# Performance work log

Measured on AMD Instinct MI355X. Metric: run time of the kernel, lower is better.

## Reference

```python
import jax, jax.numpy as jnp
import numpy as np

EPS = 1e-6
TEMP_GEO = 0.07
W_LOCAL = 0.5
W_SHARP = 0.5


def _l2norm(x):
    return x / jnp.clip(jnp.linalg.norm(x, axis=-1, keepdims=True), 1e-12)


def setup_inputs() -> dict:
    key = jax.random.key(0)
    ks = jax.random.split(key, 6)
    B, L, S, C = 8, 1024, 1024, 128
    N, P = 8, 256
    q_geo = _l2norm(jax.random.normal(ks[0], (B, L, C), jnp.float32))
    geo_pos = _l2norm(jax.random.normal(ks[1], (B, S, C), jnp.float32))
    label = jax.random.randint(ks[2], (B, L, S), 0, 2, jnp.int32)
    q_cl = jax.random.normal(ks[3], (N, P, C), jnp.float32)
    cl_pos = jax.random.normal(ks[4], (N, P, C), jnp.float32)
    idx = jax.random.randint(ks[5], (N,), 0, P, jnp.int32)
    return {"q_geo": q_geo, "q_cl": q_cl, "geo_pos": geo_pos,
            "cl_pos": cl_pos, "label": label, "idx": idx}


def _masked_mean(v, m):
    # per-sample mean over the [L,S] plane of entries where m is True
    m = m.astype(v.dtype)
    return jnp.sum(v * m, axis=(1, 2)) / jnp.maximum(jnp.sum(m, axis=(1, 2)), 1.0)


def _loftr_loss(conf, label):
    # standard LoFTR coarse CE loss (LoFTRLoss source absent from repo snippet)
    conf = jnp.clip(conf, EPS, 1.0 - EPS)
    pos = label == 1
    neg = label == 0
    pos_loss = _masked_mean(-jnp.log(conf), pos)          # [B]
    neg_loss = _masked_mean(-jnp.log(1.0 - conf), neg)    # [B]
    loss = pos_loss + neg_loss
    return jnp.mean(loss), jnp.mean(pos_loss), jnp.mean(neg_loss)


def _geometric_loss(q, k, label):
    sim = jnp.einsum('blc,bsc->bls', q, k) / TEMP_GEO        # [B,L,S]
    conf = jax.nn.softmax(sim, axis=1) * jax.nn.softmax(sim, axis=2)
    return _loftr_loss(conf, label)


def _sharpness_loss(q, k, label):
    sim = (1.0 + jnp.einsum('blc,bsc->bls', q, k)) / 2.0     # [B,L,S]
    # column stats (over L, dim=0 per sample) -> sharpness1 [B,S]
    s1 = (jnp.max(sim, axis=1) - jnp.mean(sim, axis=1)) / jnp.std(sim, axis=1, ddof=1)
    sharp1 = jax.nn.softmax(s1, axis=-1)
    # row stats (over S, dim=1 per sample) -> sharpness2 [B,L]
    s2 = (jnp.max(sim, axis=2) - jnp.mean(sim, axis=2)) / jnp.std(sim, axis=2, ddof=1)
    sharp2 = jax.nn.softmax(s2, axis=-1)
    simc = jnp.clip(sim, EPS, 1.0 - EPS)
    nll = -jnp.log(simc)
    pos = (label == 1).astype(simc.dtype)
    neg = (label == 0)
    loss1 = jnp.sum(nll * sharp1[:, None, :] * pos, axis=(1, 2))   # [B]
    loss2 = jnp.sum(nll * sharp2[:, :, None] * pos, axis=(1, 2))   # [B]
    loss3 = _masked_mean(-jnp.log(1.0 - simc), neg)                # [B]
    losses = (loss1 + loss2) / 2.0 + loss3
    return sharp1, jnp.mean(losses)


def _contrast_loss(q, all_k):
    # intended math of GeCoContrast: full cosine matrix, diag positives, tail negatives
    N = q.shape[0]
    sim = (1.0 + _l2norm(q) @ _l2norm(all_k).T) / 2.0   # [N, M]
    sim = jnp.clip(sim, EPS, 1.0 - EPS)
    l_pos = jnp.diagonal(sim[:, :N])                    # [N]
    l_neg = sim[:, N:]                                  # [N, M-N]
    return (jnp.mean(-jnp.log(l_pos)) + jnp.mean(-jnp.log(1.0 - l_neg))) / 2.0


def _forward(q_geo, q_cl, geo_pos, cl_pos, label, idx):
    loss_geo, geo_pos_loss, geo_neg_loss = _geometric_loss(q_geo, geo_pos, label)
    sharpness, loss_sharp = _sharpness_loss(q_geo, geo_pos, label)
    loss_geo = ((1.0 - W_SHARP) * loss_geo + W_SHARP * loss_sharp) * W_LOCAL

    N, P, C = q_cl.shape
    ar = jnp.arange(N)
    q_sel = q_cl[ar, idx]                               # [N,C]
    sel = cl_pos[ar, idx]                               # [N,C] positives moved to slot 0
    first = cl_pos[:, 0, :]
    swapped = cl_pos.at[ar, idx].set(first).at[:, 0, :].set(sel)
    cl_pos_save = sel
    all_k = jnp.concatenate([swapped[:, 0, :],
                             swapped[:, 1:, :].reshape(N * (P - 1), C)], axis=0)
    loss_cl = _contrast_loss(q_sel, all_k) * (1.0 - W_LOCAL)

    total = loss_geo + loss_cl
    return (sharpness, cl_pos_save, total, geo_pos_loss, geo_neg_loss, loss_sharp, loss_cl)


def reference(q_geo, q_cl, geo_pos, cl_pos, label, idx):
    return _forward(q_geo, q_cl, geo_pos, cl_pos, label, idx)
```

## Files before the change

kernel.cpp:

```cpp
#include <hip/hip_runtime.h>
#include <math.h>

#define BB 8
#define LL 1024
#define SS 1024
#define CC 128
#define NN 8
#define PP 256

static constexpr float EPS       = 1e-6f;
static constexpr float ONE_M_EPS = 1.0f - 1e-6f;
static constexpr float INV_T     = 1.0f / 0.07f;
static constexpr float NLL_MAX   = 13.815511f;
static constexpr float NLL_MIN   = 1.0000005e-6f;

static constexpr size_t DOTSZ      = (size_t)BB * LL * SS;
static constexpr size_t OFF_LSER   = DOTSZ;
static constexpr size_t OFF_LSEC   = DOTSZ + 16384;
static constexpr size_t OFF_SHARP2 = DOTSZ + 32768;
static constexpr size_t OFF_RP     = DOTSZ + 40960;
static constexpr size_t OFF_CP     = OFF_RP + 524288;
static constexpr size_t OFF_ACC    = OFF_CP + 524288;
static constexpr size_t OFF_ACCCL  = OFF_ACC + 48;
static constexpr size_t OFF_QN     = OFF_ACC + 64;
static constexpr size_t OFF_ASP    = OFF_ACC + 2048;
static constexpr size_t OFF_BSP    = OFF_ASP + 1048576;

static constexpr int OUT_CLSAVE = 8192;
static constexpr int OUT_SCAL   = 9216;

typedef __bf16 bf16x8 __attribute__((ext_vector_type(8)));
typedef float  floatx4 __attribute__((ext_vector_type(4)));

__device__ __forceinline__ void split_f4(float4 x,
                                         unsigned& hp0, unsigned& hp1,
                                         unsigned& lp0, unsigned& lp1) {
    unsigned u0 = __builtin_bit_cast(unsigned, x.x);
    unsigned u1 = __builtin_bit_cast(unsigned, x.y);
    unsigned u2 = __builtin_bit_cast(unsigned, x.z);
    unsigned u3 = __builtin_bit_cast(unsigned, x.w);
    unsigned r0 = u0 + 0x7FFFu + ((u0 >> 16) & 1u);
    unsigned r1 = u1 + 0x7FFFu + ((u1 >> 16) & 1u);
    unsigned r2 = u2 + 0x7FFFu + ((u2 >> 16) & 1u);
    unsigned r3 = u3 + 0x7FFFu + ((u3 >> 16) & 1u);
    float s0 = x.x - __builtin_bit_cast(float, r0 & 0xFFFF0000u);
    float s1 = x.y - __builtin_bit_cast(float, r1 & 0xFFFF0000u);
    float s2 = x.z - __builtin_bit_cast(float, r2 & 0xFFFF0000u);
    float s3 = x.w - __builtin_bit_cast(float, r3 & 0xFFFF0000u);
    hp0 = __builtin_amdgcn_perm(r1, r0, 0x07060302u);
    hp1 = __builtin_amdgcn_perm(r3, r2, 0x07060302u);
    lp0 = __builtin_amdgcn_perm(__builtin_bit_cast(unsigned, s1),
                                __builtin_bit_cast(unsigned, s0), 0x07060302u);
    lp1 = __builtin_amdgcn_perm(__builtin_bit_cast(unsigned, s3),
                                __builtin_bit_cast(unsigned, s2), 0x07060302u);
}

__global__ __launch_bounds__(256) void presplit(const float* __restrict__ A,
                                                const float* __restrict__ Bm,
                                                const float* __restrict__ q_cl,
                                                const float* __restrict__ cl_pos,
                                                const int* __restrict__ idx,
                                                float* __restrict__ out,
                                                float* __restrict__ ws) {
    int tid = threadIdx.x;
    if (blockIdx.x == 1024) {
        int lane = tid & 63, w = tid >> 6;
        if (tid < 52) ws[OFF_ACC + tid] = 0.0f;
        for (int n = w; n < NN; n += 4) {
            int in = idx[n];
            const float* q = q_cl + ((size_t)(n * PP + in)) * CC;
            float2 qv = *(const float2*)(q + 2 * lane);
            float ss = qv.x * qv.x + qv.y * qv.y;
            for (int o = 32; o; o >>= 1) ss += __shfl_xor(ss, o);
            float inv = 1.0f / fmaxf(sqrtf(ss), 1e-12f);
            *(float2*)(ws + OFF_QN + n * 128 + 2 * lane) = make_float2(qv.x * inv, qv.y * inv);
            const float* cp = cl_pos + ((size_t)(n * PP + in)) * CC;
            float2 cv = *(const float2*)(cp + 2 * lane);
            *(float2*)(out + OUT_CLSAVE + n * 128 + 2 * lane) = cv;
        }
        return;
    }
    int bb  = blockIdx.x;
    int mat = bb >> 9;
    size_t grow = (size_t)(bb & 511) * 16 + (tid >> 4);
    int c   = tid & 15;
    const float* in = (mat ? Bm : A) + grow * CC + c * 8;
    float4 v0 = *(const float4*)in;
    float4 v1 = *(const float4*)(in + 4);
    unsigned h0, h1, l0, l1, h2, h3, l2, l3;
    split_f4(v0, h0, h1, l0, l1);
    split_f4(v1, h2, h3, l2, l3);
    float* outp = ws + (mat ? OFF_BSP : OFF_ASP) + grow * 128 + (size_t)(c >> 2) * 32 + (c & 3) * 4;
    *(uint4*)outp        = make_uint4(h0, h1, h2, h3);
    *(uint4*)(outp + 16) = make_uint4(l0, l1, l2, l3);
}

__global__ __launch_bounds__(256, 2) void gemm_dot(float* __restrict__ dot,
                                                   float* __restrict__ ws) {
    __shared__ __align__(16) char lds[2][32768];

    int tid  = threadIdx.x;
    int lane = tid & 63;
    int w    = tid >> 6;

    int t  = blockIdx.x;
    int b  = t >> 6;
    int rm = t & 63;
    int bl = rm >> 3, bs = rm & 7;
    int R0 = bl * 128, C0 = bs * 128;

    const float* Ab = ws + OFF_ASP + ((size_t)(b * 1024 + R0)) * 128;
    const float* Bb = ws + OFF_BSP + ((size_t)(b * 1024 + C0)) * 128;

    const float* srcp[8];
    int ldsb[8];
#pragma unroll
    for (int i = 0; i < 8; i++) {
        int g   = i * 256 + tid;
        int mat = g >> 10;
        int r   = (g >> 3) & 127;
        int pc  = g & 7;
        int c   = pc ^ (r & 7);
        srcp[i] = (mat ? Bb : Ab) + (size_t)r * 128 + (c >> 2) * 16 + (c & 3) * 4;
        ldsb[i] = g * 16;
    }

    int fl   = lane & 15;
    int quad = lane >> 4;
    int wr   = w >> 1, wc = w & 1;
    int Rw   = wr * 64, Cw = wc * 64;

    floatx4 acc[4][4];
#pragma unroll
    for (int i = 0; i < 4; i++)
#pragma unroll
        for (int j = 0; j < 4; j++) acc[i][j] = (floatx4){0.f, 0.f, 0.f, 0.f};

    uint4 rg[8];
#pragma unroll
    for (int i = 0; i < 8; i++) rg[i] = *(const uint4*)(srcp[i]);
#pragma unroll
    for (int i = 0; i < 8; i++) *(uint4*)(&lds[0][ldsb[i]]) = rg[i];
    __syncthreads();

    for (int ks = 0; ks < 4; ks++) {
        int cur = ks & 1;
        if (ks < 3) {
#pragma unroll
            for (int i = 0; i < 8; i++)
                rg[i] = *(const uint4*)(srcp[i] + (ks + 1) * 32);
        }
        const char* la = lds[cur];
        const char* lb = lds[cur] + 16384;
        bf16x8 ah[4], al[4];
#pragma unroll
        for (int mt = 0; mt < 4; mt++) {
            int row = Rw + mt * 16 + fl;
            int sw  = row & 7;
            ah[mt] = *(const bf16x8*)(la + row * 128 + ((quad ^ sw) * 16));
            al[mt] = *(const bf16x8*)(la + row * 128 + (((quad + 4) ^ sw) * 16));
        }
#pragma unroll
        for (int nt = 0; nt < 4; nt++) {
            int row = Cw + nt * 16 + fl;
            int sw  = row & 7;
            bf16x8 bh  = *(const bf16x8*)(lb + row * 128 + ((quad ^ sw) * 16));
            bf16x8 blo = *(const bf16x8*)(lb + row * 128 + (((quad + 4) ^ sw) * 16));
#pragma unroll
            for (int mt = 0; mt < 4; mt++) {
                acc[mt][nt] = __builtin_amdgcn_mfma_f32_16x16x32_bf16(ah[mt], bh,  acc[mt][nt], 0, 0, 0);
                acc[mt][nt] = __builtin_amdgcn_mfma_f32_16x16x32_bf16(ah[mt], blo, acc[mt][nt], 0, 0, 0);
                acc[mt][nt] = __builtin_amdgcn_mfma_f32_16x16x32_bf16(al[mt], bh,  acc[mt][nt], 0, 0, 0);
            }
        }
        if (ks < 3) {
            char* nxt = lds[cur ^ 1];
#pragma unroll
            for (int i = 0; i < 8; i++) *(uint4*)(&nxt[ldsb[i]]) = rg[i];
        }
        __syncthreads();
    }

#pragma unroll
    for (int mt = 0; mt < 4; mt++)
#pragma unroll
        for (int nt = 0; nt < 4; nt++) {
            int col = C0 + Cw + nt * 16 + fl;
#pragma unroll
            for (int r = 0; r < 4; r++) {
                int row = R0 + Rw + mt * 16 + quad * 4 + r;
                dot[((size_t)(b * 1024 + row)) * 1024 + col] = acc[mt][nt][r];
            }
        }

    int stile = bs * 2 + wc;
    int ltile = bl * 2 + wr;
    float ces[4], cmx[4], csm[4], csq[4];
#pragma unroll
    for (int nt = 0; nt < 4; nt++) { ces[nt] = 0.f; cmx[nt] = -1e30f; csm[nt] = 0.f; csq[nt] = 0.f; }
#pragma unroll
    for (int mt = 0; mt < 4; mt++) {
#pragma unroll
        for (int r = 0; r < 4; r++) {
            float es = 0.f, mx = -1e30f, sm = 0.f, sq = 0.f;
#pragma unroll
            for (int nt = 0; nt < 4; nt++) {
                float d  = acc[mt][nt][r];
                float e  = __expf(d * INV_T);
                float s2 = fmaf(0.5f, d, 0.5f);
                es += e; mx = fmaxf(mx, s2); sm += s2; sq += s2 * s2;
                ces[nt] += e; cmx[nt] = fmaxf(cmx[nt], s2); csm[nt] += s2; csq[nt] += s2 * s2;
            }
            for (int o = 1; o < 16; o <<= 1) {
                es += __shfl_xor(es, o);
                mx = fmaxf(mx, __shfl_xor(mx, o));
                sm += __shfl_xor(sm, o);
                sq += __shfl_xor(sq, o);
            }
            if (fl == 0) {
                int row = R0 + Rw + mt * 16 + quad * 4 + r;
                *(float4*)(ws + OFF_RP + (((size_t)(b * 16 + stile)) * 1024 + row) * 4) =
                    make_float4(es, mx, sm, sq);
            }
        }
    }
#pragma unroll
    for (int nt = 0; nt < 4; nt++) {
        float es = ces[nt], mx = cmx[nt], sm = csm[nt], sq = csq[nt];
        for (int o = 16; o < 64; o <<= 1) {
            es += __shfl_xor(es, o);
            mx = fmaxf(mx, __shfl_xor(mx, o));
            sm += __shfl_xor(sm, o);
            sq += __shfl_xor(sq, o);
        }
        if (quad == 0) {
            int col = C0 + Cw + nt * 16 + fl;
            *(float4*)(ws + OFF_CP + (((size_t)(b * 16 + ltile)) * 1024 + col) * 4) =
                make_float4(es, mx, sm, sq);
        }
    }
}

__global__ __launch_bounds__(256) void mid(const float* __restrict__ cl_pos,
                                           const int* __restrict__ idx,
                                           float* __restrict__ ws,
                                           float* __restrict__ out) {
    int q   = blockIdx.x;
    int tid = threadIdx.x;
    int lane = tid & 63, wid = tid >> 6;

    if (q < 16) {
        bool docol = (q < 8);
        int b = q & 7;
        const float* part = ws + (docol ? OFF_CP : OFF_RP);
        float* lse = ws + (docol ? OFF_LSEC : OFF_LSER) + (size_t)b * 1024;
        float zs[4];
        float mxall = -1e30f;
#pragma unroll
        for (int r = 0; r < 4; r++) {
            int i = tid + r * 256;
            float es = 0.f, mx = -1e30f, sm = 0.f, sq = 0.f;
#pragma unroll
            for (int t = 0; t < 16; t++) {
                float4 v = *(const float4*)(part + (((size_t)(b * 16 + t)) * 1024 + i) * 4);
                es += v.x; mx = fmaxf(mx, v.y); sm += v.z; sq += v.w;
            }
            float mean = sm * (1.0f / 1024.0f);
            float var  = (sq - sm * sm * (1.0f / 1024.0f)) * (1.0f / 1023.0f);
            zs[r] = (mx - mean) / sqrtf(fmaxf(var, 1e-30f));
            mxall = fmaxf(mxall, zs[r]);
            lse[i] = __logf(es);
        }
        __shared__ float sb[4];
        __shared__ float red;
        float mx = mxall;
        for (int o = 32; o; o >>= 1) mx = fmaxf(mx, __shfl_xor(mx, o));
        if (!lane) sb[wid] = mx;
        __syncthreads();
        if (tid == 0) red = fmaxf(fmaxf(sb[0], sb[1]), fmaxf(sb[2], sb[3]));
        __syncthreads();
        mx = red;
        float e[4]; float smv = 0.f;
#pragma unroll
        for (int r = 0; r < 4; r++) { e[r] = __expf(zs[r] - mx); smv += e[r]; }
        for (int o = 32; o; o >>= 1) smv += __shfl_xor(smv, o);
        __syncthreads();
        if (!lane) sb[wid] = smv;
        __syncthreads();
        if (tid == 0) red = sb[0] + sb[1] + sb[2] + sb[3];
        __syncthreads();
        float inv = 1.0f / red;
        float* dst = docol ? (out + (size_t)b * 1024) : (ws + OFF_SHARP2 + (size_t)b * 1024);
#pragma unroll
        for (int r = 0; r < 4; r++) dst[tid + r * 256] = e[r] * inv;
    } else {
        int j = (q - 16) * 4 + wid;
        int m, p;
        if (j < NN) {
            m = j; p = idx[j];
        } else {
            int jj = j - NN;
            m = jj / (PP - 1);
            p = 1 + (jj - m * (PP - 1));
            if (p == idx[m]) p = 0;
        }
        const float* k = cl_pos + ((size_t)(m * PP + p)) * CC;
        float2 kv = *(const float2*)(k + 2 * lane);
        float ksq = kv.x * kv.x + kv.y * kv.y;
        for (int o = 32; o; o >>= 1) ksq += __shfl_xor(ksq, o);
        float invkn = 1.0f / fmaxf(sqrtf(ksq), 1e-12f);
        float pos = 0.0f, neg = 0.0f;
        if (j < NN) {
            const float2 qv = *(const float2*)(ws + OFF_QN + j * 128 + 2 * lane);
            float dt = qv.x * kv.x + qv.y * kv.y;
            for (int o = 32; o; o >>= 1) dt += __shfl_xor(dt, o);
            float sim = fminf(fmaxf(fmaf(0.5f * invkn, dt, 0.5f), EPS), ONE_M_EPS);
            pos = -__logf(sim);
        } else {
#pragma unroll
            for (int n = 0; n < NN; n++) {
                const float2 qv = *(const float2*)(ws + OFF_QN + n * 128 + 2 * lane);
                float dt = qv.x * kv.x + qv.y * kv.y;
                for (int o = 32; o; o >>= 1) dt += __shfl_xor(dt, o);
                float om = fminf(fmaxf(fmaf(-0.5f * invkn, dt, 0.5f), EPS), ONE_M_EPS);
                neg -= __logf(om);
            }
        }
        __shared__ float cb[2][4];
        if (!lane) { cb[0][wid] = pos; cb[1][wid] = neg; }
        __syncthreads();
        if (tid == 0) {
            float ps = cb[0][0] + cb[0][1] + cb[0][2] + cb[0][3];
            float ng = cb[1][0] + cb[1][1] + cb[1][2] + cb[1][3];
            if (ps != 0.0f) atomicAdd(ws + OFF_ACCCL + 0, ps);
            if (ng != 0.0f) atomicAdd(ws + OFF_ACCCL + 1, ng);
        }
    }
}

__device__ __forceinline__ void proc_elem(float d, int lab, float lcj, float sh1j,
                                          float lr, float s2v,
                                          float& posg, float& negg, float& l1, float& l2,
                                          float& negs, float& pcf) {
    float t = lr + lcj - d * (2.0f * INV_T);
    float isPos = (lab == 1) ? 1.0f : 0.0f;
    float isNeg = 1.0f - isPos;
    float tp   = fminf(fmaxf(t, NLL_MIN), NLL_MAX);
    float simc = fminf(fmaxf(fmaf(0.5f, d, 0.5f), EPS), ONE_M_EPS);
    float om   = fminf(fmaxf(fmaf(-0.5f, d, 0.5f), EPS), ONE_M_EPS);
    float nll2 = -__logf(simc);
    float cf   = fminf(fmaxf(__expf(-t), EPS), ONE_M_EPS);
    float nllg = -__logf(1.0f - cf);
    float nlls = -__logf(om);
    posg += isPos * tp;
    l1   += isPos * nll2 * sh1j;
    l2   += isPos * nll2 * s2v;
    pcf  += isPos;
    negg += isNeg * nllg;
    negs += isNeg * nlls;
}

__global__ __launch_bounds__(256) void main_loss(const float* __restrict__ dot,
                                                 const int* __restrict__ label,
                                                 const float* __restrict__ sharp1,
                                                 float* __restrict__ ws) {
    int b = blockIdx.y;
    int l0 = blockIdx.x * 4;
    int s = threadIdx.x * 4;
    float4 lc4 = *(const float4*)(ws + OFF_LSEC + (size_t)b * 1024 + s);
    float4 sh1 = *(const float4*)(sharp1 + (size_t)b * 1024 + s);
    const float* lser = ws + OFF_LSER + (size_t)b * 1024;
    const float* sh2  = ws + OFF_SHARP2 + (size_t)b * 1024;
    float posg = 0, negg = 0, l1 = 0, l2 = 0, negs = 0, pcf = 0;
#pragma unroll
    for (int r = 0; r < 4; r++) {
        int l = l0 + r;
        float lr  = lser[l];
        float s2v = sh2[l];
        size_t base = ((size_t)(b * 1024 + l)) * 1024 + s;
        float4 d4 = *(const float4*)(dot + base);
        int4  lb  = *(const int4*)(label + base);
        proc_elem(d4.x, lb.x, lc4.x, sh1.x, lr, s2v, posg, negg, l1, l2, negs, pcf);
        proc_elem(d4.y, lb.y, lc4.y, sh1.y, lr, s2v, posg, negg, l1, l2, negs, pcf);
        proc_elem(d4.z, lb.z, lc4.z, sh1.z, lr, s2v, posg, negg, l1, l2, negs, pcf);
        proc_elem(d4.w, lb.w, lc4.w, sh1.w, lr, s2v, posg, negg, l1, l2, negs, pcf);
    }
    float vals[6] = {posg, negg, l1, l2, negs, pcf};
    __shared__ float sb[6][4];
    int lane = threadIdx.x & 63, wid = threadIdx.x >> 6;
#pragma unroll
    for (int k = 0; k < 6; k++) {
        float v = vals[k];
        for (int o = 32; o; o >>= 1) v += __shfl_xor(v, o);
        if (!lane) sb[k][wid] = v;
    }
    __syncthreads();
    if (threadIdx.x < 6) {
        float r = sb[threadIdx.x][0] + sb[threadIdx.x][1] + sb[threadIdx.x][2] + sb[threadIdx.x][3];
        atomicAdd(ws + OFF_ACC + (size_t)b * 6 + threadIdx.x, r);
    }
}

__global__ void finalize(float* __restrict__ out, const float* __restrict__ ws) {
    if (threadIdx.x != 0) return;
    float gp = 0, gn = 0, lsh = 0;
    for (int b = 0; b < 8; b++) {
        const float* a = ws + OFF_ACC + (size_t)b * 6;
        float pc = a[5];
        float nc = (float)((size_t)LL * SS) - pc;
        gp += a[0] / fmaxf(pc, 1.0f);
        gn += a[1] / fmaxf(nc, 1.0f);
        lsh += (a[2] + a[3]) * 0.5f + a[4] / fmaxf(nc, 1.0f);
    }
    gp *= 0.125f; gn *= 0.125f; lsh *= 0.125f;
    float lgeo = gp + gn;
    float lgw = (0.5f * lgeo + 0.5f * lsh) * 0.5f;
    float clp = ws[OFF_ACCCL + 0] / 8.0f;
    float cln = ws[OFF_ACCCL + 1] / (8.0f * 2040.0f);
    float lcl = (clp + cln) * 0.5f * 0.5f;
    out[OUT_SCAL + 0] = lgw + lcl;
    out[OUT_SCAL + 1] = gp;
    out[OUT_SCAL + 2] = gn;
    out[OUT_SCAL + 3] = lsh;
    out[OUT_SCAL + 4] = lcl;
}

extern "C" void kernel_launch(void* const* d_in, const int* in_sizes, int n_in,
                              void* d_out, int out_size, void* d_ws, size_t ws_size,
                              hipStream_t stream) {
    const float* q_geo   = (const float*)d_in[0];
    const float* q_cl    = (const float*)d_in[1];
    const float* geo_pos = (const float*)d_in[2];
    const float* cl_pos  = (const float*)d_in[3];
    const int*   label   = (const int*)d_in[4];
    const int*   idx     = (const int*)d_in[5];
    float* out = (float*)d_out;
    float* ws  = (float*)d_ws;
    float* dot = ws;

    presplit<<<dim3(1025), dim3(256), 0, stream>>>(q_geo, geo_pos, q_cl, cl_pos, idx, out, ws);
    gemm_dot<<<dim3(512), dim3(256), 0, stream>>>(dot, ws);
    mid<<<dim3(528), dim3(256), 0, stream>>>(cl_pos, idx, ws, out);
    main_loss<<<dim3(256, 8), dim3(256), 0, stream>>>(dot, label, out, ws);
    finalize<<<dim3(1), dim3(64), 0, stream>>>(out, ws);
}
```

Measured before the change: 151.9 us.

## Fuse bf16 hi/lo split into GEMM tile loads, dropping presplit kernel

Removes the separate presplit kernel that wrote bf16 hi/lo copies of both operands to workspace. The GEMM now loads fp32 rows directly, splits them in registers while staging into LDS, and keeps the swizzled layout. The small q_cl normalization and accumulator-zeroing work moves to an extra block of the GEMM launch. This saves one launch and the round trip of the split operands through memory, at the cost of redundant split arithmetic since each tile is reloaded by 8 blocks.

```diff
diff --git a/kernel.cpp b/kernel.cpp
--- a/kernel.cpp
+++ b/kernel.cpp
@@ -23,8 +23,6 @@
 static constexpr size_t OFF_ACC    = OFF_CP + 524288;
 static constexpr size_t OFF_ACCCL  = OFF_ACC + 48;
 static constexpr size_t OFF_QN     = OFF_ACC + 64;
-static constexpr size_t OFF_ASP    = OFF_ACC + 2048;
-static constexpr size_t OFF_BSP    = OFF_ASP + 1048576;
 
 static constexpr int OUT_CLSAVE = 8192;
 static constexpr int OUT_SCAL   = 9216;
@@ -55,16 +53,21 @@
                                 __builtin_bit_cast(unsigned, s2), 0x07060302u);
 }
 
-__global__ __launch_bounds__(256) void presplit(const float* __restrict__ A,
-                                                const float* __restrict__ Bm,
-                                                const float* __restrict__ q_cl,
-                                                const float* __restrict__ cl_pos,
-                                                const int* __restrict__ idx,
-                                                float* __restrict__ out,
-                                                float* __restrict__ ws) {
-    int tid = threadIdx.x;
-    if (blockIdx.x == 1024) {
-        int lane = tid & 63, w = tid >> 6;
+__global__ __launch_bounds__(256, 2) void gemm_dot(const float* __restrict__ A,
+                                                   const float* __restrict__ Bm,
+                                                   const float* __restrict__ q_cl,
+                                                   const float* __restrict__ cl_pos,
+                                                   const int* __restrict__ idx,
+                                                   float* __restrict__ out,
+                                                   float* __restrict__ dot,
+                                                   float* __restrict__ ws) {
+    __shared__ __align__(16) char lds[2][32768];
+
+    int tid  = threadIdx.x;
+    int lane = tid & 63;
+    int w    = tid >> 6;
+
+    if (blockIdx.x == 512) {
         if (tid < 52) ws[OFF_ACC + tid] = 0.0f;
         for (int n = w; n < NN; n += 4) {
             int in = idx[n];
@@ -80,28 +83,6 @@
         }
         return;
     }
-    int bb  = blockIdx.x;
-    int mat = bb >> 9;
-    size_t grow = (size_t)(bb & 511) * 16 + (tid >> 4);
-    int c   = tid & 15;
-    const float* in = (mat ? Bm : A) + grow * CC + c * 8;
-    float4 v0 = *(const float4*)in;
-    float4 v1 = *(const float4*)(in + 4);
-    unsigned h0, h1, l0, l1, h2, h3, l2, l3;
-    split_f4(v0, h0, h1, l0, l1);
-    split_f4(v1, h2, h3, l2, l3);
-    float* outp = ws + (mat ? OFF_BSP : OFF_ASP) + grow * 128 + (size_t)(c >> 2) * 32 + (c & 3) * 4;
-    *(uint4*)outp        = make_uint4(h0, h1, h2, h3);
-    *(uint4*)(outp + 16) = make_uint4(l0, l1, l2, l3);
-}
-
-__global__ __launch_bounds__(256, 2) void gemm_dot(float* __restrict__ dot,
-                                                   float* __restrict__ ws) {
-    __shared__ __align__(16) char lds[2][32768];
-
-    int tid  = threadIdx.x;
-    int lane = tid & 63;
-    int w    = tid >> 6;
 
     int t  = blockIdx.x;
     int b  = t >> 6;
@@ -109,20 +90,22 @@
     int bl = rm >> 3, bs = rm & 7;
     int R0 = bl * 128, C0 = bs * 128;
 
-    const float* Ab = ws + OFF_ASP + ((size_t)(b * 1024 + R0)) * 128;
-    const float* Bb = ws + OFF_BSP + ((size_t)(b * 1024 + C0)) * 128;
-
-    const float* srcp[8];
-    int ldsb[8];
-#pragma unroll
-    for (int i = 0; i < 8; i++) {
-        int g   = i * 256 + tid;
-        int mat = g >> 10;
-        int r   = (g >> 3) & 127;
-        int pc  = g & 7;
-        int c   = pc ^ (r & 7);
-        srcp[i] = (mat ? Bb : Ab) + (size_t)r * 128 + (c >> 2) * 16 + (c & 3) * 4;
-        ldsb[i] = g * 16;
+    const float* Ab = A  + ((size_t)(b * 1024 + R0)) * CC;
+    const float* Bb = Bm + ((size_t)(b * 1024 + C0)) * CC;
+
+    const float* srcu[4];
+    int hib[4], lob[4];
+#pragma unroll
+    for (int u = 0; u < 4; u++) {
+        int g   = u * 256 + tid;
+        int mat = g >> 9;
+        int r   = (g >> 2) & 127;
+        int c8  = g & 3;
+        srcu[u] = (mat ? Bb : Ab) + (size_t)r * CC + c8 * 8;
+        int base = mat * 16384 + r * 128;
+        int sw   = r & 7;
+        hib[u] = base + ((c8 ^ sw) * 16);
+        lob[u] = base + (((c8 + 4) ^ sw) * 16);
     }
 
     int fl   = lane & 15;
@@ -136,19 +119,30 @@
 #pragma unroll
         for (int j = 0; j < 4; j++) acc[i][j] = (floatx4){0.f, 0.f, 0.f, 0.f};
 
-    uint4 rg[8];
-#pragma unroll
-    for (int i = 0; i < 8; i++) rg[i] = *(const uint4*)(srcp[i]);
-#pragma unroll
-    for (int i = 0; i < 8; i++) *(uint4*)(&lds[0][ldsb[i]]) = rg[i];
+    float4 v0[4], v1[4];
+#pragma unroll
+    for (int u = 0; u < 4; u++) {
+        v0[u] = *(const float4*)(srcu[u]);
+        v1[u] = *(const float4*)(srcu[u] + 4);
+    }
+#pragma unroll
+    for (int u = 0; u < 4; u++) {
+        unsigned h0, h1, h2, h3, l0, l1, l2, l3;
+        split_f4(v0[u], h0, h1, l0, l1);
+        split_f4(v1[u], h2, h3, l2, l3);
+        *(uint4*)(&lds[0][hib[u]]) = make_uint4(h0, h1, h2, h3);
+        *(uint4*)(&lds[0][lob[u]]) = make_uint4(l0, l1, l2, l3);
+    }
     __syncthreads();
 
     for (int ks = 0; ks < 4; ks++) {
         int cur = ks & 1;
         if (ks < 3) {
 #pragma unroll
-            for (int i = 0; i < 8; i++)
-                rg[i] = *(const uint4*)(srcp[i] + (ks + 1) * 32);
+            for (int u = 0; u < 4; u++) {
+                v0[u] = *(const float4*)(srcu[u] + (ks + 1) * 32);
+                v1[u] = *(const float4*)(srcu[u] + (ks + 1) * 32 + 4);
+            }
         }
         const char* la = lds[cur];
         const char* lb = lds[cur] + 16384;
@@ -176,7 +170,13 @@
         if (ks < 3) {
             char* nxt = lds[cur ^ 1];
 #pragma unroll
-            for (int i = 0; i < 8; i++) *(uint4*)(&nxt[ldsb[i]]) = rg[i];
+            for (int u = 0; u < 4; u++) {
+                unsigned h0, h1, h2, h3, l0, l1, l2, l3;
+                split_f4(v0[u], h0, h1, l0, l1);
+                split_f4(v1[u], h2, h3, l2, l3);
+                *(uint4*)(&nxt[hib[u]]) = make_uint4(h0, h1, h2, h3);
+                *(uint4*)(&nxt[lob[u]]) = make_uint4(l0, l1, l2, l3);
+            }
         }
         __syncthreads();
     }
@@ -438,8 +438,7 @@
     float* ws  = (float*)d_ws;
     float* dot = ws;
 
-    presplit<<<dim3(1025), dim3(256), 0, stream>>>(q_geo, geo_pos, q_cl, cl_pos, idx, out, ws);
-    gemm_dot<<<dim3(512), dim3(256), 0, stream>>>(dot, ws);
+    gemm_dot<<<dim3(513), dim3(256), 0, stream>>>(q_geo, geo_pos, q_cl, cl_pos, idx, out, dot, ws);
     mid<<<dim3(528), dim3(256), 0, stream>>>(cl_pos, idx, ws, out);
     main_loss<<<dim3(256, 8), dim3(256), 0, stream>>>(dot, label, out, ws);
     finalize<<<dim3(1), dim3(64), 0, stream>>>(out, ws);
```

Result: faster. 148.6 us (-2.2%).
